# Optimization experiments

Hardware: AMD Instinct MI355X
Metric: run time of the kernel (lower is better)

## Reference

```python
import jax, jax.numpy as jnp
import numpy as np

N_LEVELS = 16
F_PER = 2
T = 1 << 19            # hashmap size per level
BASE = 16
FINE = 2048
PLS = np.exp(np.log(FINE / BASE) / (N_LEVELS - 1))  # per-level scale
PRIMES = (1, 2654435761, 805459861)                  # tcnn hash primes
# 8 corner offsets of the trilinear cell, bit d of corner i -> axis d offset
OFFSETS = np.array([[(i >> d) & 1 for d in range(3)] for i in range(8)], dtype=np.uint32)
N_RAYS = 2_097_152


def hash_grid_encode(x, table):
    """Instant-NGP style multires hash encoding with smoothstep interpolation.
    x: [N,3] in [0,1]; table: [L,T,F]. Returns [N, L*F]."""
    offs = jnp.asarray(OFFSETS)                      # [8,3] uint32
    offs_b = jnp.asarray(OFFSETS.astype(bool))       # [8,3] bool
    outs = []
    for l in range(N_LEVELS):
        scale = BASE * (PLS ** l) - 1.0              # grid scale (static python float)
        res = int(np.ceil(scale)) + 1                # grid resolution at this level
        pos = x * jnp.float32(scale) + 0.5           # [N,3]
        ipos = jnp.floor(pos)
        f = pos - ipos                               # fractional part in [0,1)
        w = f * f * (3.0 - 2.0 * f)                  # smoothstep weights
        c = ipos.astype(jnp.uint32)[:, None, :] + offs[None]   # [N,8,3] corner coords
        if res ** 3 <= T:
            # dense grid fits in the table slice
            idx = c[..., 0] + c[..., 1] * jnp.uint32(res) + c[..., 2] * jnp.uint32(res * res)
        else:
            # spatial hash (wrapping uint32 arithmetic), T is a power of two
            idx = (c[..., 0] * jnp.uint32(PRIMES[0])) ^ \
                  (c[..., 1] * jnp.uint32(PRIMES[1])) ^ \
                  (c[..., 2] * jnp.uint32(PRIMES[2]))
            idx = idx & jnp.uint32(T - 1)
        feat = table[l][idx.astype(jnp.int32)]       # [N,8,F] gather
        # trilinear corner weights: prod over axes of w or (1-w)
        wc = jnp.prod(jnp.where(offs_b[None], w[:, None, :], 1.0 - w[:, None, :]), axis=-1)  # [N,8]
        outs.append(jnp.einsum('nc,ncf->nf', wc, feat))
    return jnp.concatenate(outs, axis=-1)            # [N, L*F]


def setup_inputs() -> dict:
    key = jax.random.key(0)
    ks = jax.random.split(key, 6)
    d = jax.random.normal(ks[0], (N_RAYS, 3), dtype=jnp.float32)
    d = d / jnp.linalg.norm(d, axis=-1, keepdims=True)         # unit directions
    table = jax.random.uniform(ks[1], (N_LEVELS, T, F_PER), jnp.float32, -1e-4, 1e-4)
    dim_in = N_LEVELS * F_PER + 3                               # 35
    W1 = jax.random.normal(ks[2], (dim_in, 64), jnp.float32) * (1.0 / np.sqrt(dim_in))
    W2 = jax.random.normal(ks[3], (64, 64), jnp.float32) * (1.0 / 8.0)
    W3 = jax.random.normal(ks[4], (64, 1), jnp.float32) * (1.0 / 8.0)
    return {"directions": d, "table": table,
            "W1": W1, "b1": jnp.zeros((64,), jnp.float32),
            "W2": W2, "b2": jnp.zeros((64,), jnp.float32),
            "W3": W3, "b3": jnp.zeros((1,), jnp.float32)}


def reference(directions, table, W1, b1, W2, b2, W3, b3):
    dir_scaled = directions * 0.49 + 0.49                       # map to [0,1] cube
    feat = hash_grid_encode(dir_scaled, table)                  # [N,32]
    h = jnp.concatenate([directions, feat], axis=-1)            # [N,35]
    h = jax.nn.relu(h @ W1 + b1)
    h = jax.nn.relu(h @ W2 + b2)
    out = h @ W3 + b3                                           # [N,1]
    distance = jax.nn.softplus(out[..., 0] + 1.0)               # [N]
    return distance
```

## Files before the change

### kernel.cpp

```cpp
#include <hip/hip_runtime.h>
#include <hip/hip_bf16.h>
#include <cmath>

#define NL 16
#define TSIZE (1u << 19)
#define TMASK (TSIZE - 1u)
#define NBINS (1u << 18)

typedef __attribute__((ext_vector_type(8))) short bf16x8;
typedef __attribute__((ext_vector_type(4))) float f32x4;

struct LevelParams {
  float scale[NL];
  unsigned res[NL];
  unsigned dense_mask;
};

static __device__ __forceinline__ short f2bf(float f) {
  __hip_bfloat16 h = __float2bfloat16(f);
  return *reinterpret_cast<short*>(&h);
}
static __device__ __forceinline__ short lo16(unsigned u) { return (short)(u & 0xffffu); }
static __device__ __forceinline__ short hi16(unsigned u) { return (short)(u >> 16); }

static __device__ __forceinline__ unsigned spread3(unsigned x) {
  x &= 0x3FFu;
  x = (x | (x << 16)) & 0x030000FFu;
  x = (x | (x << 8))  & 0x0300F00Fu;
  x = (x | (x << 4))  & 0x030C30C3u;
  x = (x | (x << 2))  & 0x09249249u;
  return x;
}
static __device__ __forceinline__ unsigned ray_key(float dx, float dy, float dz) {
  float X0 = dx * 0.49f + 0.49f;
  float X1 = dy * 0.49f + 0.49f;
  float X2 = dz * 0.49f + 0.49f;
  unsigned qx = (unsigned)(X0 * 64.0f); qx = qx > 63u ? 63u : qx;
  unsigned qy = (unsigned)(X1 * 64.0f); qy = qy > 63u ? 63u : qy;
  unsigned qz = (unsigned)(X2 * 64.0f); qz = qz > 63u ? 63u : qz;
  return spread3(qx) | (spread3(qy) << 1) | (spread3(qz) << 2);
}

__global__ __launch_bounds__(256)
void histidx_k(const float* __restrict__ dirs, unsigned* __restrict__ hist,
               unsigned* __restrict__ keyidx, int n) {
  int i = blockIdx.x * 256 + threadIdx.x;
  if (i >= n) return;
  unsigned key = ray_key(dirs[i * 3 + 0], dirs[i * 3 + 1], dirs[i * 3 + 2]);
  unsigned idx = atomicAdd(&hist[key], 1u);
  keyidx[i] = key | (idx << 18);
}

__global__ __launch_bounds__(256)
void scanA_k(unsigned* __restrict__ hist, unsigned* __restrict__ blockSums) {
  __shared__ unsigned sums[256];
  int bid = blockIdx.x, t = threadIdx.x;
  unsigned base = (unsigned)bid * 1024u + (unsigned)t * 4u;
  uint4 c = *(uint4*)&hist[base];
  unsigned s = c.x + c.y + c.z + c.w;
  sums[t] = s;
  __syncthreads();
  for (int off = 1; off < 256; off <<= 1) {
    unsigned v = (t >= off) ? sums[t - off] : 0u;
    __syncthreads();
    sums[t] += v;
    __syncthreads();
  }
  unsigned excl = sums[t] - s;
  uint4 o;
  o.x = excl;
  o.y = excl + c.x;
  o.z = excl + c.x + c.y;
  o.w = excl + c.x + c.y + c.z;
  *(uint4*)&hist[base] = o;
  if (t == 255) blockSums[bid] = sums[255];
}

__global__ __launch_bounds__(256)
void scanB_k(unsigned* __restrict__ blockSums) {
  __shared__ unsigned sums[256];
  int t = threadIdx.x;
  unsigned s = blockSums[t];
  sums[t] = s;
  __syncthreads();
  for (int off = 1; off < 256; off <<= 1) {
    unsigned v = (t >= off) ? sums[t - off] : 0u;
    __syncthreads();
    sums[t] += v;
    __syncthreads();
  }
  blockSums[t] = sums[t] - s;
}

__global__ __launch_bounds__(256)
void scatter2_k(const unsigned* __restrict__ keyidx,
                const unsigned* __restrict__ hist,
                const unsigned* __restrict__ bsums,
                unsigned* __restrict__ order, int n) {
  int i = blockIdx.x * 256 + threadIdx.x;
  if (i >= n) return;
  unsigned ki = keyidx[i];
  unsigned key = ki & (NBINS - 1u);
  unsigned idx = ki >> 18;
  unsigned pos = hist[key] + bsums[key >> 10] + idx;
  order[pos] = (unsigned)i;
}

#define ROWS 72
#define FSTR 257

__global__ __launch_bounds__(256, 3)
void fused_k(const float* __restrict__ dirs,
             const float* __restrict__ table,
             const unsigned* __restrict__ order,
             const float* __restrict__ W1, const float* __restrict__ b1,
             const float* __restrict__ W2, const float* __restrict__ b2,
             const float* __restrict__ W3, const float* __restrict__ b3,
             float* __restrict__ out, int n, LevelParams lp)
{
  __shared__ unsigned FH[(4 * 32 * ROWS) / 2];
  __shared__ short W1T[64 * ROWS];
  __shared__ short W2T[64 * ROWS];
  unsigned* F  = FH;
  short*    H1 = (short*)FH;

  int tid = threadIdx.x;

  {
    int nn = tid >> 2;
    int kg = tid & 3;
    bf16x8 v1a, v1b, v2a, v2b;
    #pragma unroll
    for (int j = 0; j < 8; ++j) {
      int k0 = kg * 16 + j, k1 = kg * 16 + 8 + j;
      v1a[j] = (k0 < 32) ? f2bf(W1[(k0 + 3) * 64 + nn])
             : (k0 < 35) ? f2bf(W1[(k0 - 32) * 64 + nn]) : (short)0;
      v1b[j] = (k1 < 32) ? f2bf(W1[(k1 + 3) * 64 + nn])
             : (k1 < 35) ? f2bf(W1[(k1 - 32) * 64 + nn]) : (short)0;
      v2a[j] = f2bf(W2[k0 * 64 + nn]);
      v2b[j] = f2bf(W2[k1 * 64 + nn]);
    }
    int wo = nn * ROWS + kg * 16;
    *(bf16x8*)&W1T[wo]     = v1a;
    *(bf16x8*)&W1T[wo + 8] = v1b;
    *(bf16x8*)&W2T[wo]     = v2a;
    *(bf16x8*)&W2T[wo + 8] = v2b;
  }

  int nwg = gridDim.x;
  int bidx = blockIdx.x;
  int chunk = ((nwg & 7) == 0) ? ((bidx & 7) * (nwg >> 3) + (bidx >> 3)) : bidx;

  int ray = chunk * 256 + tid;
  int rcg = ray < n ? ray : (n - 1);
  unsigned o = order[rcg];
  float dxr = dirs[o * 3 + 0];
  float dyr = dirs[o * 3 + 1];
  float dzr = dirs[o * 3 + 2];

  float X0 = dxr * 0.49f + 0.49f;
  float X1 = dyr * 0.49f + 0.49f;
  float X2 = dzr * 0.49f + 0.49f;

  for (int l0 = 0; l0 < 8; ++l0) {
    float wa0[2][3], wa1[2][3];
    bool dns[2];
    unsigned didx[2][8];
    unsigned par[2][4];
    const float2* tb[2];

    #pragma unroll
    for (int g = 0; g < 2; ++g) {
      int level = l0 + g * 8;
      float s = lp.scale[level];
      unsigned r = lp.res[level];
      dns[g] = (lp.dense_mask >> level) & 1u;

      float px = X0 * s + 0.5f, py = X1 * s + 0.5f, pz = X2 * s + 0.5f;
      float gx = floorf(px), gy = floorf(py), gz = floorf(pz);
      float fx = px - gx, fy = py - gy, fz = pz - gz;
      unsigned ix = (unsigned)gx, iy = (unsigned)gy, iz = (unsigned)gz;

      wa1[g][0] = fx * fx * (3.0f - 2.0f * fx);
      wa1[g][1] = fy * fy * (3.0f - 2.0f * fy);
      wa1[g][2] = fz * fz * (3.0f - 2.0f * fz);
      wa0[g][0] = 1.0f - wa1[g][0];
      wa0[g][1] = 1.0f - wa1[g][1];
      wa0[g][2] = 1.0f - wa1[g][2];

      if (dns[g]) {
        unsigned r2 = r * r;
        unsigned x0 = ix, x1 = ix + 1u;
        unsigned y0 = iy * r, y1 = y0 + r;
        unsigned z0 = iz * r2, z1 = z0 + r2;
        didx[g][0] = x0 + y0 + z0; didx[g][1] = x1 + y0 + z0;
        didx[g][2] = x0 + y1 + z0; didx[g][3] = x1 + y1 + z0;
        didx[g][4] = x0 + y0 + z1; didx[g][5] = x1 + y0 + z1;
        didx[g][6] = x0 + y1 + z1; didx[g][7] = x1 + y1 + z1;
      } else {
        unsigned y0 = iy * 2654435761u, y1 = y0 + 2654435761u;
        unsigned z0 = iz * 805459861u,  z1 = z0 + 805459861u;
        unsigned p0 = (ix ^ y0 ^ z0) & TMASK;
        unsigned p1 = (ix ^ y1 ^ z0) & TMASK;
        unsigned p2 = (ix ^ y0 ^ z1) & TMASK;
        unsigned p3 = (ix ^ y1 ^ z1) & TMASK;
        didx[g][0] = p0 >> 1; didx[g][1] = p1 >> 1;
        didx[g][2] = p2 >> 1; didx[g][3] = p3 >> 1;
        par[g][0] = p0 & 1u; par[g][1] = p1 & 1u;
        par[g][2] = p2 & 1u; par[g][3] = p3 & 1u;
      }
      tb[g] = (const float2*)table + (size_t)level * TSIZE;
    }

    float2 v[2][8];
    float4 f4[2][4];
    #pragma unroll
    for (int g = 0; g < 2; ++g) {
      if (dns[g]) {
        #pragma unroll
        for (int c = 0; c < 8; ++c) v[g][c] = tb[g][didx[g][c]];
      } else {
        const float4* t4p = (const float4*)tb[g];
        #pragma unroll
        for (int c = 0; c < 4; ++c) f4[g][c] = t4p[didx[g][c]];
      }
    }
    #pragma unroll
    for (int g = 0; g < 2; ++g) {
      if (!dns[g]) {
        #pragma unroll
        for (int c = 0; c < 4; ++c) {
          float2 even, odd;
          even.x = f4[g][c].x; even.y = f4[g][c].y;
          odd.x  = f4[g][c].z; odd.y  = f4[g][c].w;
          bool od = par[g][c] != 0;
          v[g][2 * c]     = od ? odd : even;
          v[g][2 * c + 1] = od ? even : odd;
        }
      }
    }

    #pragma unroll
    for (int g = 0; g < 2; ++g) {
      float wx0 = wa0[g][0], wx1 = wa1[g][0];
      float wy0 = wa0[g][1], wy1 = wa1[g][1];
      float wz0 = wa0[g][2], wz1 = wa1[g][2];
      float wy0z0 = wy0 * wz0, wy1z0 = wy1 * wz0, wy0z1 = wy0 * wz1, wy1z1 = wy1 * wz1;
      float w000 = wx0 * wy0z0, w100 = wx1 * wy0z0;
      float w010 = wx0 * wy1z0, w110 = wx1 * wy1z0;
      float w001 = wx0 * wy0z1, w101 = wx1 * wy0z1;
      float w011 = wx0 * wy1z1, w111 = wx1 * wy1z1;

      float a0 = w000 * v[g][0].x + w100 * v[g][1].x + w010 * v[g][2].x + w110 * v[g][3].x
               + w001 * v[g][4].x + w101 * v[g][5].x + w011 * v[g][6].x + w111 * v[g][7].x;
      float a1 = w000 * v[g][0].y + w100 * v[g][1].y + w010 * v[g][2].y + w110 * v[g][3].y
               + w001 * v[g][4].y + w101 * v[g][5].y + w011 * v[g][6].y + w111 * v[g][7].y;

      int level = l0 + g * 8;
      unsigned packed = ((unsigned)f2bf(a0) & 0xffffu) | (((unsigned)f2bf(a1) & 0xffffu) << 16);
      F[level * FSTR + tid] = packed;
    }
  }
  __syncthreads();

  int wave = tid >> 6, lane = tid & 63;
  int q = lane >> 4, nl = lane & 15;

  float b1v[4], b2v[4], w3v[4];
  #pragma unroll
  for (int t4 = 0; t4 < 4; ++t4) {
    b1v[t4] = b1[t4 * 16 + nl];
    b2v[t4] = b2[t4 * 16 + nl];
    w3v[t4] = W3[t4 * 16 + nl];
  }
  float b3s = b3[0];

  bf16x8 a0h[2][2];
  #pragma unroll
  for (int batch = 0; batch < 2; ++batch) {
    #pragma unroll
    for (int t = 0; t < 2; ++t) {
      int rl = wave * 64 + batch * 32 + t * 16 + nl;
      unsigned u0 = F[(q * 4 + 0) * FSTR + rl];
      unsigned u1 = F[(q * 4 + 1) * FSTR + rl];
      unsigned u2 = F[(q * 4 + 2) * FSTR + rl];
      unsigned u3 = F[(q * 4 + 3) * FSTR + rl];
      a0h[batch][t][0] = lo16(u0); a0h[batch][t][1] = hi16(u0);
      a0h[batch][t][2] = lo16(u1); a0h[batch][t][3] = hi16(u1);
      a0h[batch][t][4] = lo16(u2); a0h[batch][t][5] = hi16(u2);
      a0h[batch][t][6] = lo16(u3); a0h[batch][t][7] = hi16(u3);
    }
  }
  __syncthreads();

  #pragma unroll
  for (int batch = 0; batch < 2; ++batch) {
    int lbase = wave * 64 + batch * 32;

    bf16x8 a1[2];
    #pragma unroll
    for (int t = 0; t < 2; ++t) {
      a1[t][0] = 0; a1[t][1] = 0; a1[t][2] = 0; a1[t][3] = 0;
      a1[t][4] = 0; a1[t][5] = 0; a1[t][6] = 0; a1[t][7] = 0;
      int sl = batch * 32 + t * 16 + nl;
      float sdx = __shfl(dxr, sl, 64);
      float sdy = __shfl(dyr, sl, 64);
      float sdz = __shfl(dzr, sl, 64);
      if (q == 0) {
        a1[t][0] = f2bf(sdx);
        a1[t][1] = f2bf(sdy);
        a1[t][2] = f2bf(sdz);
      }
    }

    f32x4 acc[2][4];
    #pragma unroll
    for (int t4 = 0; t4 < 4; ++t4) {
      int brow = (t4 * 16 + nl) * ROWS;
      bf16x8 bt0 = *(const bf16x8*)&W1T[brow + q * 8];
      bf16x8 bt1 = *(const bf16x8*)&W1T[brow + 32 + q * 8];
      #pragma unroll
      for (int t = 0; t < 2; ++t) {
        f32x4 z = {0.f, 0.f, 0.f, 0.f};
        z = __builtin_amdgcn_mfma_f32_16x16x32_bf16(a0h[batch][t], bt0, z, 0, 0, 0);
        z = __builtin_amdgcn_mfma_f32_16x16x32_bf16(a1[t], bt1, z, 0, 0, 0);
        acc[t][t4] = z;
      }
    }
    #pragma unroll
    for (int t = 0; t < 2; ++t)
      #pragma unroll
      for (int t4 = 0; t4 < 4; ++t4)
        #pragma unroll
        for (int i = 0; i < 4; ++i) {
          float v = fmaxf(acc[t][t4][i] + b1v[t4], 0.0f);
          H1[wave * (32 * ROWS) + (t * 16 + q * 4 + i) * ROWS + t4 * 16 + nl] = f2bf(v);
        }
    __syncthreads();

    #pragma unroll
    for (int t4 = 0; t4 < 4; ++t4) {
      int brow = (t4 * 16 + nl) * ROWS;
      bf16x8 bt0 = *(const bf16x8*)&W2T[brow + q * 8];
      bf16x8 bt1 = *(const bf16x8*)&W2T[brow + 32 + q * 8];
      #pragma unroll
      for (int t = 0; t < 2; ++t) {
        bf16x8 h0  = *(const bf16x8*)&H1[wave * (32 * ROWS) + (t * 16 + nl) * ROWS + q * 8];
        bf16x8 h1f = *(const bf16x8*)&H1[wave * (32 * ROWS) + (t * 16 + nl) * ROWS + 32 + q * 8];
        f32x4 z = {0.f, 0.f, 0.f, 0.f};
        z = __builtin_amdgcn_mfma_f32_16x16x32_bf16(h0, bt0, z, 0, 0, 0);
        z = __builtin_amdgcn_mfma_f32_16x16x32_bf16(h1f, bt1, z, 0, 0, 0);
        acc[t][t4] = z;
      }
    }

    #pragma unroll
    for (int t = 0; t < 2; ++t) {
      float part[4] = {0.f, 0.f, 0.f, 0.f};
      #pragma unroll
      for (int t4 = 0; t4 < 4; ++t4)
        #pragma unroll
        for (int i = 0; i < 4; ++i) {
          float v = fmaxf(acc[t][t4][i] + b2v[t4], 0.0f);
          part[i] = fmaf(v, w3v[t4], part[i]);
        }
      #pragma unroll
      for (int s = 1; s < 16; s <<= 1) {
        #pragma unroll
        for (int i = 0; i < 4; ++i) part[i] += __shfl_xor(part[i], s, 64);
      }
      unsigned oi[4];
      #pragma unroll
      for (int i = 0; i < 4; ++i)
        oi[i] = __shfl(o, batch * 32 + t * 16 + q * 4 + i, 64);
      if (nl == 0) {
        int orow = chunk * 256 + lbase + t * 16 + q * 4;
        #pragma unroll
        for (int i = 0; i < 4; ++i) {
          if (orow + i < n) {
            float v = part[i] + b3s + 1.0f;
            out[oi[i]] = fmaxf(v, 0.0f) + log1pf(expf(-fabsf(v)));
          }
        }
      }
    }
    __syncthreads();
  }
}

extern "C" void kernel_launch(void* const* d_in, const int* in_sizes, int n_in,
                              void* d_out, int out_size, void* d_ws, size_t ws_size,
                              hipStream_t stream) {
  const float* dirs  = (const float*)d_in[0];
  const float* table = (const float*)d_in[1];
  const float* W1 = (const float*)d_in[2];
  const float* b1 = (const float*)d_in[3];
  const float* W2 = (const float*)d_in[4];
  const float* b2 = (const float*)d_in[5];
  const float* W3 = (const float*)d_in[6];
  const float* b3 = (const float*)d_in[7];
  float* out = (float*)d_out;
  int n = in_sizes[0] / 3;

  LevelParams lp;
  double pls = std::exp(std::log(2048.0 / 16.0) / 15.0);
  unsigned dm = 0;
  for (int l = 0; l < NL; ++l) {
    double scale = 16.0 * std::pow(pls, (double)l) - 1.0;
    lp.scale[l] = (float)scale;
    long long res = (long long)std::ceil(scale) + 1;
    lp.res[l] = (unsigned)res;
    if (res * res * res <= (long long)TSIZE) dm |= (1u << l);
  }
  lp.dense_mask = dm;

  size_t order_bytes  = (size_t)n * 4;
  size_t keyidx_bytes = (size_t)n * 4;
  size_t hist_bytes   = (size_t)NBINS * 4;

  int blocks256 = (n + 255) / 256;

  char* base = (char*)d_ws;
  unsigned* order  = (unsigned*)base;
  unsigned* keyidx = (unsigned*)(base + order_bytes);
  unsigned* hist   = (unsigned*)(base + order_bytes + keyidx_bytes);
  unsigned* bsums  = (unsigned*)(base + order_bytes + keyidx_bytes + hist_bytes);

  hipMemsetAsync(hist, 0, hist_bytes, stream);
  hipLaunchKernelGGL(histidx_k, dim3(blocks256), dim3(256), 0, stream,
                     dirs, hist, keyidx, n);
  hipLaunchKernelGGL(scanA_k, dim3(256), dim3(256), 0, stream, hist, bsums);
  hipLaunchKernelGGL(scanB_k, dim3(1), dim3(256), 0, stream, bsums);
  hipLaunchKernelGGL(scatter2_k, dim3(blocks256), dim3(256), 0, stream,
                     keyidx, hist, bsums, order, n);
  hipLaunchKernelGGL(fused_k, dim3(blocks256), dim3(256), 0, stream,
                     dirs, table, order, W1, b1, W2, b2, W3, b3, out, n, lp);
}
```

Measured before the change: 612.2 us.

## Merge sort preprocessing kernels into one cooperative kernel with grid syncs

Replaces the memset, histogram, two scan kernels and scatter kernel with a single cooperative launch of 1024 blocks that uses grid.sync between phases. The aim is to remove several kernel launch gaps and a memset from the ray-sorting preprocessing. In exchange, each phase runs on a fixed grid that loops over rays, and grid-wide barriers add their own cost. The old multi-kernel path is kept as a fallback if the cooperative launch fails.

```diff
diff --git a/kernel.cpp b/kernel.cpp
--- a/kernel.cpp
+++ b/kernel.cpp
@@ -1,6 +1,9 @@
 #include <hip/hip_runtime.h>
 #include <hip/hip_bf16.h>
+#include <hip/hip_cooperative_groups.h>
 #include <cmath>
+
+namespace cg = cooperative_groups;
 
 #define NL 16
 #define TSIZE (1u << 19)
@@ -39,6 +42,73 @@
   unsigned qy = (unsigned)(X1 * 64.0f); qy = qy > 63u ? 63u : qy;
   unsigned qz = (unsigned)(X2 * 64.0f); qz = qz > 63u ? 63u : qz;
   return spread3(qx) | (spread3(qy) << 1) | (spread3(qz) << 2);
+}
+
+__global__ __launch_bounds__(256)
+void sort_coop(const float* __restrict__ dirs,
+               unsigned* __restrict__ hist,
+               unsigned* __restrict__ keyidx,
+               unsigned* __restrict__ bsums,
+               unsigned* __restrict__ order, int n)
+{
+  cg::grid_group grid = cg::this_grid();
+  __shared__ unsigned sums[256];
+  int b = blockIdx.x, t = threadIdx.x;
+  int gtid = b * 256 + t;
+  int gsize = gridDim.x * 256;
+
+  for (int i = gtid; i < (int)NBINS; i += gsize) hist[i] = 0u;
+  grid.sync();
+
+  for (int i = gtid; i < n; i += gsize) {
+    unsigned key = ray_key(dirs[i * 3 + 0], dirs[i * 3 + 1], dirs[i * 3 + 2]);
+    unsigned idx = atomicAdd(&hist[key], 1u);
+    keyidx[i] = key | (idx << 18);
+  }
+  grid.sync();
+
+  {
+    unsigned c = hist[b * 256 + t];
+    sums[t] = c;
+    __syncthreads();
+    for (int off = 1; off < 256; off <<= 1) {
+      unsigned v = (t >= off) ? sums[t - off] : 0u;
+      __syncthreads();
+      sums[t] += v;
+      __syncthreads();
+    }
+    hist[b * 256 + t] = sums[t] - c;
+    if (t == 255) bsums[b] = sums[255];
+  }
+  grid.sync();
+
+  if (b == 0) {
+    unsigned v0 = bsums[t * 4 + 0], v1 = bsums[t * 4 + 1];
+    unsigned v2 = bsums[t * 4 + 2], v3 = bsums[t * 4 + 3];
+    unsigned s = v0 + v1 + v2 + v3;
+    sums[t] = s;
+    __syncthreads();
+    for (int off = 1; off < 256; off <<= 1) {
+      unsigned v = (t >= off) ? sums[t - off] : 0u;
+      __syncthreads();
+      sums[t] += v;
+      __syncthreads();
+    }
+    unsigned excl = sums[t] - s;
+    bsums[t * 4 + 0] = excl;
+    bsums[t * 4 + 1] = excl + v0;
+    bsums[t * 4 + 2] = excl + v0 + v1;
+    bsums[t * 4 + 3] = excl + v0 + v1 + v2;
+  }
+  grid.sync();
+
+  for (int i = gtid; i < n; i += gsize) {
+    unsigned ki = keyidx[i];
+    unsigned key = ki & (NBINS - 1u);
+    unsigned idx = ki >> 18;
+    unsigned pos = hist[key] + bsums[key >> 8] + idx;
+    order[pos] = (unsigned)i;
+  }
 }
 
 __global__ __launch_bounds__(256)
@@ -426,13 +496,20 @@
   unsigned* hist   = (unsigned*)(base + order_bytes + keyidx_bytes);
   unsigned* bsums  = (unsigned*)(base + order_bytes + keyidx_bytes + hist_bytes);
 
-  hipMemsetAsync(hist, 0, hist_bytes, stream);
-  hipLaunchKernelGGL(histidx_k, dim3(blocks256), dim3(256), 0, stream,
-                     dirs, hist, keyidx, n);
-  hipLaunchKernelGGL(scanA_k, dim3(256), dim3(256), 0, stream, hist, bsums);
-  hipLaunchKernelGGL(scanB_k, dim3(1), dim3(256), 0, stream, bsums);
-  hipLaunchKernelGGL(scatter2_k, dim3(blocks256), dim3(256), 0, stream,
-                     keyidx, hist, bsums, order, n);
+  void* cargs[] = {(void*)&dirs, (void*)&hist, (void*)&keyidx,
+                   (void*)&bsums, (void*)&order, (void*)&n};
+  hipError_t cerr = hipLaunchCooperativeKernel((const void*)sort_coop,
+                                               dim3(1024), dim3(256),
+                                               cargs, 0, stream);
+  if (cerr != hipSuccess) {
+    hipMemsetAsync(hist, 0, hist_bytes, stream);
+    hipLaunchKernelGGL(histidx_k, dim3(blocks256), dim3(256), 0, stream,
+                       dirs, hist, keyidx, n);
+    hipLaunchKernelGGL(scanA_k, dim3(256), dim3(256), 0, stream, hist, bsums);
+    hipLaunchKernelGGL(scanB_k, dim3(1), dim3(256), 0, stream, bsums);
+    hipLaunchKernelGGL(scatter2_k, dim3(blocks256), dim3(256), 0, stream,
+                       keyidx, hist, bsums, order, n);
+  }
   hipLaunchKernelGGL(fused_k, dim3(blocks256), dim3(256), 0, stream,
                      dirs, table, order, W1, b1, W2, b2, W3, b3, out, n, lp);
 }
```

Measured after the change: 999.1 us. 63.2% more time.

## Split hash-grid levels across two threads per ray, 128 rays per block

Applied to the files above, without the earlier changes.

Each block now handles 128 rays with two threads per ray, and each thread encodes 8 of the 16 levels instead of all 16. The MLP stage processes one batch of 32 rows per wave instead of two, which drops a loop iteration and a barrier. The grid doubles in size. This exposes more parallel gathers and shortens each thread's serial chain of dependent table loads. The cost is more redundant per-block work (weight staging into LDS, order and direction loads) per ray, and wave-level shuffles now read from interleaved lanes.

```diff
diff --git a/kernel.cpp b/kernel.cpp
--- a/kernel.cpp
+++ b/kernel.cpp
@@ -107,7 +107,7 @@
 }
 
 #define ROWS 72
-#define FSTR 257
+#define FSTR2 130
 
 __global__ __launch_bounds__(256, 3)
 void fused_k(const float* __restrict__ dirs,
@@ -151,7 +151,9 @@
   int bidx = blockIdx.x;
   int chunk = ((nwg & 7) == 0) ? ((bidx & 7) * (nwg >> 3) + (bidx >> 3)) : bidx;
 
-  int ray = chunk * 256 + tid;
+  int rpos = tid >> 1;
+  int h = tid & 1;
+  int ray = chunk * 128 + rpos;
   int rcg = ray < n ? ray : (n - 1);
   unsigned o = order[rcg];
   float dxr = dirs[o * 3 + 0];
@@ -162,7 +164,11 @@
   float X1 = dyr * 0.49f + 0.49f;
   float X2 = dzr * 0.49f + 0.49f;
 
-  for (int l0 = 0; l0 < 8; ++l0) {
+  for (int j = 0; j < 4; ++j) {
+    int lv[2];
+    lv[0] = h * 8 + j;
+    lv[1] = h * 8 + j + 4;
+
     float wa0[2][3], wa1[2][3];
     bool dns[2];
     unsigned didx[2][8];
@@ -171,7 +177,7 @@
 
     #pragma unroll
     for (int g = 0; g < 2; ++g) {
-      int level = l0 + g * 8;
+      int level = lv[g];
       float s = lp.scale[level];
       unsigned r = lp.res[level];
       dns[g] = (lp.dense_mask >> level) & 1u;
@@ -256,9 +262,8 @@
       float a1 = w000 * v[g][0].y + w100 * v[g][1].y + w010 * v[g][2].y + w110 * v[g][3].y
                + w001 * v[g][4].y + w101 * v[g][5].y + w011 * v[g][6].y + w111 * v[g][7].y;
 
-      int level = l0 + g * 8;
       unsigned packed = ((unsigned)f2bf(a0) & 0xffffu) | (((unsigned)f2bf(a1) & 0xffffu) << 16);
-      F[level * FSTR + tid] = packed;
+      F[lv[g] * FSTR2 + rpos] = packed;
     }
   }
   __syncthreads();
@@ -275,34 +280,28 @@
   }
   float b3s = b3[0];
 
-  bf16x8 a0h[2][2];
+  bf16x8 a0h[2];
   #pragma unroll
-  for (int batch = 0; batch < 2; ++batch) {
-    #pragma unroll
-    for (int t = 0; t < 2; ++t) {
-      int rl = wave * 64 + batch * 32 + t * 16 + nl;
-      unsigned u0 = F[(q * 4 + 0) * FSTR + rl];
-      unsigned u1 = F[(q * 4 + 1) * FSTR + rl];
-      unsigned u2 = F[(q * 4 + 2) * FSTR + rl];
-      unsigned u3 = F[(q * 4 + 3) * FSTR + rl];
-      a0h[batch][t][0] = lo16(u0); a0h[batch][t][1] = hi16(u0);
-      a0h[batch][t][2] = lo16(u1); a0h[batch][t][3] = hi16(u1);
-      a0h[batch][t][4] = lo16(u2); a0h[batch][t][5] = hi16(u2);
-      a0h[batch][t][6] = lo16(u3); a0h[batch][t][7] = hi16(u3);
-    }
+  for (int t = 0; t < 2; ++t) {
+    int rl = wave * 32 + t * 16 + nl;
+    unsigned u0 = F[(q * 4 + 0) * FSTR2 + rl];
+    unsigned u1 = F[(q * 4 + 1) * FSTR2 + rl];
+    unsigned u2 = F[(q * 4 + 2) * FSTR2 + rl];
+    unsigned u3 = F[(q * 4 + 3) * FSTR2 + rl];
+    a0h[t][0] = lo16(u0); a0h[t][1] = hi16(u0);
+    a0h[t][2] = lo16(u1); a0h[t][3] = hi16(u1);
+    a0h[t][4] = lo16(u2); a0h[t][5] = hi16(u2);
+    a0h[t][6] = lo16(u3); a0h[t][7] = hi16(u3);
   }
   __syncthreads();
 
-  #pragma unroll
-  for (int batch = 0; batch < 2; ++batch) {
-    int lbase = wave * 64 + batch * 32;
-
+  {
     bf16x8 a1[2];
     #pragma unroll
     for (int t = 0; t < 2; ++t) {
       a1[t][0] = 0; a1[t][1] = 0; a1[t][2] = 0; a1[t][3] = 0;
       a1[t][4] = 0; a1[t][5] = 0; a1[t][6] = 0; a1[t][7] = 0;
-      int sl = batch * 32 + t * 16 + nl;
+      int sl = 2 * (t * 16 + nl);
       float sdx = __shfl(dxr, sl, 64);
       float sdy = __shfl(dyr, sl, 64);
       float sdz = __shfl(dzr, sl, 64);
@@ -322,7 +321,7 @@
       #pragma unroll
       for (int t = 0; t < 2; ++t) {
         f32x4 z = {0.f, 0.f, 0.f, 0.f};
-        z = __builtin_amdgcn_mfma_f32_16x16x32_bf16(a0h[batch][t], bt0, z, 0, 0, 0);
+        z = __builtin_amdgcn_mfma_f32_16x16x32_bf16(a0h[t], bt0, z, 0, 0, 0);
         z = __builtin_amdgcn_mfma_f32_16x16x32_bf16(a1[t], bt1, z, 0, 0, 0);
         acc[t][t4] = z;
       }
@@ -372,9 +371,9 @@
       unsigned oi[4];
       #pragma unroll
       for (int i = 0; i < 4; ++i)
-        oi[i] = __shfl(o, batch * 32 + t * 16 + q * 4 + i, 64);
+        oi[i] = __shfl(o, 2 * (t * 16 + q * 4 + i), 64);
       if (nl == 0) {
-        int orow = chunk * 256 + lbase + t * 16 + q * 4;
+        int orow = chunk * 128 + wave * 32 + t * 16 + q * 4;
         #pragma unroll
         for (int i = 0; i < 4; ++i) {
           if (orow + i < n) {
@@ -384,7 +383,6 @@
         }
       }
     }
-    __syncthreads();
   }
 }
 
@@ -419,6 +417,7 @@
   size_t hist_bytes   = (size_t)NBINS * 4;
 
   int blocks256 = (n + 255) / 256;
+  int blocks128 = (n + 127) / 128;
 
   char* base = (char*)d_ws;
   unsigned* order  = (unsigned*)base;
@@ -433,6 +432,6 @@
   hipLaunchKernelGGL(scanB_k, dim3(1), dim3(256), 0, stream, bsums);
   hipLaunchKernelGGL(scatter2_k, dim3(blocks256), dim3(256), 0, stream,
                      keyidx, hist, bsums, order, n);
-  hipLaunchKernelGGL(fused_k, dim3(blocks256), dim3(256), 0, stream,
+  hipLaunchKernelGGL(fused_k, dim3(blocks128), dim3(256), 0, stream,
                      dirs, table, order, W1, b1, W2, b2, W3, b3, out, n, lp);
 }
```

Result: slower. 734.0 us (+19.9%).
